# Kernel tuning notes

Hardware: AMD Instinct MI355X
Metric: run time of the kernel (lower is better)

The kernel has to match this reference:

```python
import jax, jax.numpy as jnp
import numpy as np

B, S, D, H, E = 2, 2048, 1024, 2048, 8


def setup_inputs() -> dict:
    key = jax.random.key(0)
    ks = jax.random.split(key, 5)
    scale_in = 0.02
    x = jax.random.normal(ks[0], (B, S, D), dtype=jnp.float32)
    Wr = jax.random.normal(ks[1], (D, E), dtype=jnp.float32) * scale_in
    br = jnp.zeros((E,), dtype=jnp.float32)
    W1 = jax.random.normal(ks[2], (E, D, H), dtype=jnp.float32) * (1.0 / np.sqrt(D))
    b1 = jnp.zeros((E, H), dtype=jnp.float32)
    W2 = jax.random.normal(ks[3], (E, H, D), dtype=jnp.float32) * (1.0 / np.sqrt(H))
    b2 = jnp.zeros((E, D), dtype=jnp.float32)
    return {"x": x, "Wr": Wr, "br": br, "W1": W1, "b1": b1, "W2": W2, "b2": b2, "k": 2}


def reference(x, Wr, br, W1, b1, W2, b2, k):
    # Router: top-k logits, softmax over the k selected logits
    logits = x @ Wr + br                       # [B,S,E]
    top_v, top_i = jax.lax.top_k(logits, k)    # [B,S,k]
    scores = jax.nn.softmax(top_v, axis=-1)    # [B,S,k]

    # Dense all-expert MLP (reference combine): [B,S,E,*]
    h = jax.nn.relu(jnp.einsum('bsd,edh->bseh', x, W1) + b1[None, None])
    eo = jnp.einsum('bseh,ehd->bsed', h, W2) + b2[None, None]  # [B,S,E,D]

    # Gather the k selected experts per token and combine with scores
    sel = jnp.take_along_axis(eo, top_i[..., None], axis=2)   # [B,S,k,D]
    out = jnp.sum(scores[..., None] * sel, axis=2)             # [B,S,D]
    return out
```

## Files before the change

### kernel.cpp

```cpp
#include <hip/hip_runtime.h>
#include <hip/hip_bf16.h>

#define TOKENS 4096
#define DDIM 1024
#define HDIM 2048
#define NEXP 8
#define NASSIGN 8192
#define MAX_TILES 80

typedef __attribute__((ext_vector_type(8))) __bf16 bf16x8;
typedef __attribute__((ext_vector_type(4))) float f32x4;
typedef __attribute__((ext_vector_type(4))) unsigned short u16x4;

__device__ __forceinline__ unsigned short f2bf(float f) {
    unsigned int u = __builtin_bit_cast(unsigned int, f);
    u += 0x7fffu + ((u >> 16) & 1u);
    return (unsigned short)(u >> 16);
}

__global__ __launch_bounds__(256) void router_kernel(
    const float* __restrict__ x, const float* __restrict__ Wr, const float* __restrict__ br,
    int* __restrict__ topk_e, float* __restrict__ topk_s)
{
    const int t = blockIdx.x * 4 + (threadIdx.x >> 6);
    const int lane = threadIdx.x & 63;
    const float* xr = x + (long)t * DDIM;
    float acc[8] = {0.f,0.f,0.f,0.f,0.f,0.f,0.f,0.f};
    for (int it = 0; it < DDIM / 64; ++it) {
        const int d = it * 64 + lane;
        const float xv = xr[d];
        const float4 w0 = *(const float4*)(Wr + d * 8);
        const float4 w1 = *(const float4*)(Wr + d * 8 + 4);
        acc[0] += xv * w0.x; acc[1] += xv * w0.y; acc[2] += xv * w0.z; acc[3] += xv * w0.w;
        acc[4] += xv * w1.x; acc[5] += xv * w1.y; acc[6] += xv * w1.z; acc[7] += xv * w1.w;
    }
#pragma unroll
    for (int e = 0; e < 8; ++e) {
        float v = acc[e];
        for (int off = 32; off > 0; off >>= 1) v += __shfl_down(v, off, 64);
        acc[e] = v;
    }
    if (lane == 0) {
        float lg[8];
#pragma unroll
        for (int e = 0; e < 8; ++e) lg[e] = acc[e] + br[e];
        int i0 = 0; float v0 = lg[0];
#pragma unroll
        for (int e = 1; e < 8; ++e) if (lg[e] > v0) { v0 = lg[e]; i0 = e; }
        int i1 = -1; float v1 = -3.4e38f;
#pragma unroll
        for (int e = 0; e < 8; ++e) if (e != i0 && lg[e] > v1) { v1 = lg[e]; i1 = e; }
        const float e1 = expf(v1 - v0);
        const float inv = 1.f / (1.f + e1);
        topk_e[t * 2]     = i0; topk_s[t * 2]     = inv;
        topk_e[t * 2 + 1] = i1; topk_s[t * 2 + 1] = e1 * inv;
    }
}

__global__ __launch_bounds__(256) void build_lists_kernel(
    const int* __restrict__ topk_e, const float* __restrict__ topk_s,
    int* __restrict__ token_list, float* __restrict__ score_list, int* __restrict__ meta)
{
    __shared__ int cnt[NEXP];
    __shared__ int base[NEXP];
    __shared__ int cur[NEXP];
    const int tid = threadIdx.x;
    if (tid < NEXP) cnt[tid] = 0;
    __syncthreads();
    for (int i = tid; i < NASSIGN; i += 256) atomicAdd(&cnt[topk_e[i]], 1);
    __syncthreads();
    if (tid == 0) {
        int accu = 0;
        for (int e = 0; e < NEXP; ++e) { base[e] = accu; cur[e] = accu; accu += cnt[e]; }
        int ntile = 0;
        for (int e = 0; e < NEXP; ++e) {
            const int c = cnt[e];
            for (int r = 0; r * 128 < c; ++r) {
                meta[1 + ntile] = e;
                meta[1 + MAX_TILES + ntile] = base[e] + r * 128;
                meta[1 + 2 * MAX_TILES + ntile] = (c - r * 128) < 128 ? (c - r * 128) : 128;
                ++ntile;
            }
        }
        meta[0] = ntile;
    }
    __syncthreads();
    for (int i = tid; i < NASSIGN; i += 256) {
        const int e = topk_e[i];
        const int slot = atomicAdd(&cur[e], 1);
        token_list[slot] = i >> 1;
        score_list[slot] = topk_s[i];
    }
}

__global__ __launch_bounds__(256) void convert_x_kernel(
    const float* __restrict__ src, unsigned short* __restrict__ dst)
{
    const long i = ((long)blockIdx.x * 256 + threadIdx.x) * 4;
    const float4 v = *(const float4*)(src + i);
    u16x4 o;
    o.x = f2bf(v.x); o.y = f2bf(v.y); o.z = f2bf(v.z); o.w = f2bf(v.w);
    *(u16x4*)(dst + i) = o;
}

__global__ __launch_bounds__(256) void transpose_cvt_kernel(
    const float* __restrict__ src, unsigned short* __restrict__ dst, int K, int N)
{
    __shared__ unsigned short tile[32 * 33];
    const int e = blockIdx.z;
    const int k0 = blockIdx.x * 32;
    const int n0 = blockIdx.y * 32;
    const int r = threadIdx.x >> 3;
    const int c4 = (threadIdx.x & 7) * 4;
    const float4 v = *(const float4*)(src + ((long)e * K + k0 + r) * N + n0 + c4);
    tile[(c4 + 0) * 33 + r] = f2bf(v.x);
    tile[(c4 + 1) * 33 + r] = f2bf(v.y);
    tile[(c4 + 2) * 33 + r] = f2bf(v.z);
    tile[(c4 + 3) * 33 + r] = f2bf(v.w);
    __syncthreads();
    u16x4 o;
    o.x = tile[r * 33 + c4 + 0];
    o.y = tile[r * 33 + c4 + 1];
    o.z = tile[r * 33 + c4 + 2];
    o.w = tile[r * 33 + c4 + 3];
    *(u16x4*)(dst + ((long)e * N + n0 + r) * K + k0 + c4) = o;
}

template<int KDIM, int NDIM, bool G2>
__global__ __launch_bounds__(256, 2) void expert_gemm(
    const unsigned short* __restrict__ Abase,
    const unsigned short* __restrict__ Bt,
    const float* __restrict__ bias,
    unsigned short* __restrict__ Hout,
    float* __restrict__ Out,
    const int* __restrict__ token_list,
    const float* __restrict__ score_list,
    const int* __restrict__ meta)
{
    const int nt = meta[0];
    const int bx = blockIdx.x;
    if (bx >= nt) return;
    const int e = meta[1 + bx];
    const int slot0 = meta[1 + MAX_TILES + bx];
    const int rows_valid = meta[1 + 2 * MAX_TILES + bx];
    const int n0 = blockIdx.y * 128;

    __shared__ unsigned short As[128 * 32];
    __shared__ unsigned short Bs[128 * 32];

    const int tid = threadIdx.x;
    const int lane = tid & 63;
    const int w = tid >> 6;
    const int wm = w & 1;
    const int wn = w >> 1;
    const int quad = lane >> 4;
    const int l15 = lane & 15;

    const unsigned short* aptr[2];
    const unsigned short* bptr[2];
    unsigned short* lA[2];
    unsigned short* lB[2];
#pragma unroll
    for (int c = 0; c < 2; ++c) {
        const int l16 = (c * 4 + w) * 64 + lane;
        const int row = l16 >> 2;
        const int col8 = (l16 & 3) * 8;
        const int rr = row < rows_valid ? row : rows_valid - 1;
        const long arow = G2 ? (long)(slot0 + rr) : (long)token_list[slot0 + rr];
        aptr[c] = Abase + arow * KDIM + col8;
        bptr[c] = Bt + ((long)e * NDIM + n0 + row) * (long)KDIM + col8;
        lA[c] = &As[(c * 4 + w) * 512];
        lB[c] = &Bs[(c * 4 + w) * 512];
    }

    f32x4 acc[4][4] = {};

#pragma unroll 1
    for (int k0 = 0; k0 < KDIM; k0 += 32) {
#pragma unroll
        for (int c = 0; c < 2; ++c) {
            __builtin_amdgcn_global_load_lds(
                (const __attribute__((address_space(1))) unsigned int*)aptr[c],
                (__attribute__((address_space(3))) unsigned int*)lA[c], 16, 0, 0);
            __builtin_amdgcn_global_load_lds(
                (const __attribute__((address_space(1))) unsigned int*)bptr[c],
                (__attribute__((address_space(3))) unsigned int*)lB[c], 16, 0, 0);
            aptr[c] += 32;
            bptr[c] += 32;
        }
        __syncthreads();

        bf16x8 af[4], bfr[4];
#pragma unroll
        for (int mi = 0; mi < 4; ++mi)
            af[mi] = *(const bf16x8*)&As[(wm * 64 + mi * 16 + l15) * 32 + quad * 8];
#pragma unroll
        for (int ni = 0; ni < 4; ++ni)
            bfr[ni] = *(const bf16x8*)&Bs[(wn * 64 + ni * 16 + l15) * 32 + quad * 8];
#pragma unroll
        for (int mi = 0; mi < 4; ++mi)
#pragma unroll
            for (int ni = 0; ni < 4; ++ni)
                acc[mi][ni] = __builtin_amdgcn_mfma_f32_16x16x32_bf16(af[mi], bfr[ni], acc[mi][ni], 0, 0, 0);
        __syncthreads();
    }

#pragma unroll
    for (int mi = 0; mi < 4; ++mi) {
#pragma unroll
        for (int ni = 0; ni < 4; ++ni) {
            const int col = n0 + wn * 64 + ni * 16 + l15;
#pragma unroll
            for (int r = 0; r < 4; ++r) {
                const int row = wm * 64 + mi * 16 + quad * 4 + r;
                if (row < rows_valid) {
                    float v = acc[mi][ni][r] + bias[e * NDIM + col];
                    if (!G2) {
                        v = v > 0.f ? v : 0.f;
                        Hout[(long)(slot0 + row) * NDIM + col] = f2bf(v);
                    } else {
                        const int slot = slot0 + row;
                        const int tok = token_list[slot];
                        const float s = score_list[slot];
                        unsafeAtomicAdd(&Out[(long)tok * NDIM + col], s * v);
                    }
                }
            }
        }
    }
}

extern "C" void kernel_launch(void* const* d_in, const int* in_sizes, int n_in,
                              void* d_out, int out_size, void* d_ws, size_t ws_size,
                              hipStream_t stream)
{
    (void)in_sizes; (void)n_in; (void)out_size; (void)ws_size;
    const float* x  = (const float*)d_in[0];
    const float* Wr = (const float*)d_in[1];
    const float* br = (const float*)d_in[2];
    const float* W1 = (const float*)d_in[3];
    const float* b1 = (const float*)d_in[4];
    const float* W2 = (const float*)d_in[5];
    const float* b2 = (const float*)d_in[6];
    float* out = (float*)d_out;

    char* ws = (char*)d_ws;
    unsigned short* x_bf  = (unsigned short*)(ws);
    unsigned short* W1t   = (unsigned short*)(ws + 8388608);
    unsigned short* W2t   = (unsigned short*)(ws + 41943040);
    unsigned short* hbuf  = (unsigned short*)(ws + 75497472);
    int*   topk_e     = (int*)(ws + 109051904);
    float* topk_s     = (float*)(ws + 109084672);
    int*   token_list = (int*)(ws + 109117440);
    float* score_list = (float*)(ws + 109150208);
    int*   meta       = (int*)(ws + 109182976);

    hipMemsetAsync(d_out, 0, (size_t)TOKENS * DDIM * sizeof(float), stream);

    router_kernel<<<TOKENS / 4, 256, 0, stream>>>(x, Wr, br, topk_e, topk_s);
    convert_x_kernel<<<TOKENS * DDIM / 1024, 256, 0, stream>>>(x, x_bf);
    transpose_cvt_kernel<<<dim3(DDIM / 32, HDIM / 32, NEXP), 256, 0, stream>>>(W1, W1t, DDIM, HDIM);
    transpose_cvt_kernel<<<dim3(HDIM / 32, DDIM / 32, NEXP), 256, 0, stream>>>(W2, W2t, HDIM, DDIM);
    build_lists_kernel<<<1, 256, 0, stream>>>(topk_e, topk_s, token_list, score_list, meta);
    expert_gemm<DDIM, HDIM, false><<<dim3(MAX_TILES, HDIM / 128), 256, 0, stream>>>(
        x_bf, W1t, b1, hbuf, nullptr, token_list, score_list, meta);
    expert_gemm<HDIM, DDIM, true><<<dim3(MAX_TILES, DDIM / 128), 256, 0, stream>>>(
        hbuf, W2t, b2, nullptr, out, token_list, score_list, meta);
}
```

Baseline: 407.8 us.

## Fuse x conversion into router, merge weight transposes, deepen GEMM K tile with swizzle

The x-to-bf16 conversion now happens inside the router kernel, removing one launch and one extra read of x. The two weight transpose-convert launches become a single kernel with 64x64 tiles. The list builder runs with 1024 threads. The expert GEMM now loads 64-wide K slices into XOR-swizzled LDS, which halves the number of barriers and is meant to cut bank conflicts. Tiles are also remapped so that consecutive tiles land on the same XCD, which could help L2 reuse of expert weights. Costs are twice the LDS per block and more complex indexing.

```diff
diff --git a/kernel.cpp b/kernel.cpp
--- a/kernel.cpp
+++ b/kernel.cpp
@@ -20,15 +20,17 @@
 
 __global__ __launch_bounds__(256) void router_kernel(
     const float* __restrict__ x, const float* __restrict__ Wr, const float* __restrict__ br,
-    int* __restrict__ topk_e, float* __restrict__ topk_s)
+    unsigned short* __restrict__ x_bf, int* __restrict__ topk_e, float* __restrict__ topk_s)
 {
     const int t = blockIdx.x * 4 + (threadIdx.x >> 6);
     const int lane = threadIdx.x & 63;
     const float* xr = x + (long)t * DDIM;
+    unsigned short* xo = x_bf + (long)t * DDIM;
     float acc[8] = {0.f,0.f,0.f,0.f,0.f,0.f,0.f,0.f};
     for (int it = 0; it < DDIM / 64; ++it) {
         const int d = it * 64 + lane;
         const float xv = xr[d];
+        xo[d] = f2bf(xv);
         const float4 w0 = *(const float4*)(Wr + d * 8);
         const float4 w1 = *(const float4*)(Wr + d * 8 + 4);
         acc[0] += xv * w0.x; acc[1] += xv * w0.y; acc[2] += xv * w0.z; acc[3] += xv * w0.w;
@@ -57,7 +59,7 @@
     }
 }
 
-__global__ __launch_bounds__(256) void build_lists_kernel(
+__global__ __launch_bounds__(1024) void build_lists_kernel(
     const int* __restrict__ topk_e, const float* __restrict__ topk_s,
     int* __restrict__ token_list, float* __restrict__ score_list, int* __restrict__ meta)
 {
@@ -67,7 +69,7 @@
     const int tid = threadIdx.x;
     if (tid < NEXP) cnt[tid] = 0;
     __syncthreads();
-    for (int i = tid; i < NASSIGN; i += 256) atomicAdd(&cnt[topk_e[i]], 1);
+    for (int i = tid; i < NASSIGN; i += 1024) atomicAdd(&cnt[topk_e[i]], 1);
     __syncthreads();
     if (tid == 0) {
         int accu = 0;
@@ -85,7 +87,7 @@
         meta[0] = ntile;
     }
     __syncthreads();
-    for (int i = tid; i < NASSIGN; i += 256) {
+    for (int i = tid; i < NASSIGN; i += 1024) {
         const int e = topk_e[i];
         const int slot = atomicAdd(&cur[e], 1);
         token_list[slot] = i >> 1;
@@ -93,37 +95,43 @@
     }
 }
 
-__global__ __launch_bounds__(256) void convert_x_kernel(
-    const float* __restrict__ src, unsigned short* __restrict__ dst)
-{
-    const long i = ((long)blockIdx.x * 256 + threadIdx.x) * 4;
-    const float4 v = *(const float4*)(src + i);
-    u16x4 o;
-    o.x = f2bf(v.x); o.y = f2bf(v.y); o.z = f2bf(v.z); o.w = f2bf(v.w);
-    *(u16x4*)(dst + i) = o;
-}
-
 __global__ __launch_bounds__(256) void transpose_cvt_kernel(
-    const float* __restrict__ src, unsigned short* __restrict__ dst, int K, int N)
-{
-    __shared__ unsigned short tile[32 * 33];
-    const int e = blockIdx.z;
-    const int k0 = blockIdx.x * 32;
-    const int n0 = blockIdx.y * 32;
-    const int r = threadIdx.x >> 3;
-    const int c4 = (threadIdx.x & 7) * 4;
-    const float4 v = *(const float4*)(src + ((long)e * K + k0 + r) * N + n0 + c4);
-    tile[(c4 + 0) * 33 + r] = f2bf(v.x);
-    tile[(c4 + 1) * 33 + r] = f2bf(v.y);
-    tile[(c4 + 2) * 33 + r] = f2bf(v.z);
-    tile[(c4 + 3) * 33 + r] = f2bf(v.w);
-    __syncthreads();
-    u16x4 o;
-    o.x = tile[r * 33 + c4 + 0];
-    o.y = tile[r * 33 + c4 + 1];
-    o.z = tile[r * 33 + c4 + 2];
-    o.w = tile[r * 33 + c4 + 3];
-    *(u16x4*)(dst + ((long)e * N + n0 + r) * K + k0 + c4) = o;
+    const float* __restrict__ W1, const float* __restrict__ W2,
+    unsigned short* __restrict__ W1t, unsigned short* __restrict__ W2t)
+{
+    __shared__ unsigned short tile[64 * 68];
+    const int z = blockIdx.y;
+    const bool is1 = z < 8;
+    const int e = is1 ? z : z - 8;
+    const int K = is1 ? DDIM : HDIM;
+    const int N = is1 ? HDIM : DDIM;
+    const float* src = (is1 ? W1 : W2) + (long)e * K * N;
+    unsigned short* dst = (is1 ? W1t : W2t) + (long)e * K * N;
+    const int ktiles = K >> 6;
+    const int k0 = (blockIdx.x % ktiles) * 64;
+    const int n0 = (blockIdx.x / ktiles) * 64;
+    const int r0 = threadIdx.x >> 4;
+    const int c4 = (threadIdx.x & 15) * 4;
+#pragma unroll
+    for (int i = 0; i < 4; ++i) {
+        const int r = r0 + i * 16;
+        const float4 v = *(const float4*)(src + (long)(k0 + r) * N + n0 + c4);
+        tile[(c4 + 0) * 68 + r] = f2bf(v.x);
+        tile[(c4 + 1) * 68 + r] = f2bf(v.y);
+        tile[(c4 + 2) * 68 + r] = f2bf(v.z);
+        tile[(c4 + 3) * 68 + r] = f2bf(v.w);
+    }
+    __syncthreads();
+#pragma unroll
+    for (int i = 0; i < 4; ++i) {
+        const int rn = r0 + i * 16;
+        u16x4 o;
+        o.x = tile[rn * 68 + c4 + 0];
+        o.y = tile[rn * 68 + c4 + 1];
+        o.z = tile[rn * 68 + c4 + 2];
+        o.w = tile[rn * 68 + c4 + 3];
+        *(u16x4*)(dst + (long)(n0 + rn) * K + k0 + c4) = o;
+    }
 }
 
 template<int KDIM, int NDIM, bool G2>
@@ -138,15 +146,20 @@
     const int* __restrict__ meta)
 {
     const int nt = meta[0];
-    const int bx = blockIdx.x;
-    if (bx >= nt) return;
-    const int e = meta[1 + bx];
-    const int slot0 = meta[1 + MAX_TILES + bx];
-    const int rows_valid = meta[1 + 2 * MAX_TILES + bx];
+    const int xcd = blockIdx.x & 7;
+    const int off = blockIdx.x >> 3;
+    const int q = nt >> 3;
+    const int r = nt & 7;
+    const int cnt_i = q + (xcd < r ? 1 : 0);
+    if (off >= cnt_i) return;
+    const int t = xcd * q + (xcd < r ? xcd : r) + off;
+    const int e = meta[1 + t];
+    const int slot0 = meta[1 + MAX_TILES + t];
+    const int rows_valid = meta[1 + 2 * MAX_TILES + t];
     const int n0 = blockIdx.y * 128;
 
-    __shared__ unsigned short As[128 * 32];
-    __shared__ unsigned short Bs[128 * 32];
+    __shared__ unsigned short As[128 * 64];
+    __shared__ unsigned short Bs[128 * 64];
 
     const int tid = threadIdx.x;
     const int lane = tid & 63;
@@ -156,52 +169,58 @@
     const int quad = lane >> 4;
     const int l15 = lane & 15;
 
-    const unsigned short* aptr[2];
-    const unsigned short* bptr[2];
-    unsigned short* lA[2];
-    unsigned short* lB[2];
-#pragma unroll
-    for (int c = 0; c < 2; ++c) {
-        const int l16 = (c * 4 + w) * 64 + lane;
-        const int row = l16 >> 2;
-        const int col8 = (l16 & 3) * 8;
+    const unsigned short* aptr[4];
+    const unsigned short* bptr[4];
+    unsigned short* lA[4];
+    unsigned short* lB[4];
+#pragma unroll
+    for (int c = 0; c < 4; ++c) {
+        const int chunk = c * 256 + tid;
+        const int row = chunk >> 3;
+        const int kc = (chunk & 7) ^ (row & 7);
         const int rr = row < rows_valid ? row : rows_valid - 1;
         const long arow = G2 ? (long)(slot0 + rr) : (long)token_list[slot0 + rr];
-        aptr[c] = Abase + arow * KDIM + col8;
-        bptr[c] = Bt + ((long)e * NDIM + n0 + row) * (long)KDIM + col8;
-        lA[c] = &As[(c * 4 + w) * 512];
-        lB[c] = &Bs[(c * 4 + w) * 512];
+        aptr[c] = Abase + arow * (long)KDIM + kc * 8;
+        bptr[c] = Bt + ((long)e * NDIM + n0 + row) * (long)KDIM + kc * 8;
+        lA[c] = &As[(c * 256 + w * 64) * 8];
+        lB[c] = &Bs[(c * 256 + w * 64) * 8];
     }
 
     f32x4 acc[4][4] = {};
 
 #pragma unroll 1
-    for (int k0 = 0; k0 < KDIM; k0 += 32) {
-#pragma unroll
-        for (int c = 0; c < 2; ++c) {
+    for (int k0 = 0; k0 < KDIM; k0 += 64) {
+#pragma unroll
+        for (int c = 0; c < 4; ++c) {
             __builtin_amdgcn_global_load_lds(
                 (const __attribute__((address_space(1))) unsigned int*)aptr[c],
                 (__attribute__((address_space(3))) unsigned int*)lA[c], 16, 0, 0);
+            aptr[c] += 64;
+        }
+#pragma unroll
+        for (int c = 0; c < 4; ++c) {
             __builtin_amdgcn_global_load_lds(
                 (const __attribute__((address_space(1))) unsigned int*)bptr[c],
                 (__attribute__((address_space(3))) unsigned int*)lB[c], 16, 0, 0);
-            aptr[c] += 32;
-            bptr[c] += 32;
+            bptr[c] += 64;
         }
         __syncthreads();
 
-        bf16x8 af[4], bfr[4];
-#pragma unroll
-        for (int mi = 0; mi < 4; ++mi)
-            af[mi] = *(const bf16x8*)&As[(wm * 64 + mi * 16 + l15) * 32 + quad * 8];
-#pragma unroll
-        for (int ni = 0; ni < 4; ++ni)
-            bfr[ni] = *(const bf16x8*)&Bs[(wn * 64 + ni * 16 + l15) * 32 + quad * 8];
-#pragma unroll
-        for (int mi = 0; mi < 4; ++mi)
+#pragma unroll
+        for (int h = 0; h < 2; ++h) {
+            bf16x8 af[4], bfr[4];
+#pragma unroll
+            for (int mi = 0; mi < 4; ++mi)
+                af[mi] = *(const bf16x8*)&As[(wm * 64 + mi * 16 + l15) * 64 + ((h * 4 + quad) ^ (l15 & 7)) * 8];
 #pragma unroll
             for (int ni = 0; ni < 4; ++ni)
-                acc[mi][ni] = __builtin_amdgcn_mfma_f32_16x16x32_bf16(af[mi], bfr[ni], acc[mi][ni], 0, 0, 0);
+                bfr[ni] = *(const bf16x8*)&Bs[(wn * 64 + ni * 16 + l15) * 64 + ((h * 4 + quad) ^ (l15 & 7)) * 8];
+#pragma unroll
+            for (int mi = 0; mi < 4; ++mi)
+#pragma unroll
+                for (int ni = 0; ni < 4; ++ni)
+                    acc[mi][ni] = __builtin_amdgcn_mfma_f32_16x16x32_bf16(af[mi], bfr[ni], acc[mi][ni], 0, 0, 0);
+        }
         __syncthreads();
     }
 
@@ -211,10 +230,10 @@
         for (int ni = 0; ni < 4; ++ni) {
             const int col = n0 + wn * 64 + ni * 16 + l15;
 #pragma unroll
-            for (int r = 0; r < 4; ++r) {
-                const int row = wm * 64 + mi * 16 + quad * 4 + r;
+            for (int rr = 0; rr < 4; ++rr) {
+                const int row = wm * 64 + mi * 16 + quad * 4 + rr;
                 if (row < rows_valid) {
-                    float v = acc[mi][ni][r] + bias[e * NDIM + col];
+                    float v = acc[mi][ni][rr] + bias[e * NDIM + col];
                     if (!G2) {
                         v = v > 0.f ? v : 0.f;
                         Hout[(long)(slot0 + row) * NDIM + col] = f2bf(v);
@@ -257,11 +276,9 @@
 
     hipMemsetAsync(d_out, 0, (size_t)TOKENS * DDIM * sizeof(float), stream);
 
-    router_kernel<<<TOKENS / 4, 256, 0, stream>>>(x, Wr, br, topk_e, topk_s);
-    convert_x_kernel<<<TOKENS * DDIM / 1024, 256, 0, stream>>>(x, x_bf);
-    transpose_cvt_kernel<<<dim3(DDIM / 32, HDIM / 32, NEXP), 256, 0, stream>>>(W1, W1t, DDIM, HDIM);
-    transpose_cvt_kernel<<<dim3(HDIM / 32, DDIM / 32, NEXP), 256, 0, stream>>>(W2, W2t, HDIM, DDIM);
-    build_lists_kernel<<<1, 256, 0, stream>>>(topk_e, topk_s, token_list, score_list, meta);
+    router_kernel<<<TOKENS / 4, 256, 0, stream>>>(x, Wr, br, x_bf, topk_e, topk_s);
+    build_lists_kernel<<<1, 1024, 0, stream>>>(topk_e, topk_s, token_list, score_list, meta);
+    transpose_cvt_kernel<<<dim3(512, 16), 256, 0, stream>>>(W1, W2, W1t, W2t);
     expert_gemm<DDIM, HDIM, false><<<dim3(MAX_TILES, HDIM / 128), 256, 0, stream>>>(
         x_bf, W1t, b1, hbuf, nullptr, token_list, score_list, meta);
     expert_gemm<HDIM, DDIM, true><<<dim3(MAX_TILES, DDIM / 128), 256, 0, stream>>>(
```

After: 337.5 us. 1.21x faster.
